# Performance work log

Hardware: AMD Instinct MI355X
Metric: run time of the kernel (lower is better)

## Reference

```python
import jax, jax.numpy as jnp
import numpy as np

N = 50000      # nodes
E = 800000     # edges (avg degree 16)
D_IN = 128
HID = [128, 64, 32]
C = 2
EPS = 1e-5


def _lin(k, fan_in, fan_out):
    return jax.random.normal(k, (fan_in, fan_out), jnp.float32) / np.float32(np.sqrt(fan_in))


def setup_inputs() -> dict:
    key = jax.random.key(0)
    ks = jax.random.split(key, 40)
    inp = {}
    inp["x"] = jax.random.normal(ks[0], (N, D_IN), jnp.float32)
    inp["edge_index"] = jax.random.randint(ks[1], (2, E), 0, N, dtype=jnp.int32)
    i = 2
    dims = [D_IN] + HID
    for l in range(3):
        di, do = dims[l], dims[l + 1]
        inp[f"W{l}"] = _lin(ks[i], di, do); i += 1
        inp[f"b{l}"] = jnp.zeros((do,), jnp.float32)
        inp[f"bn{l}_g"] = jnp.ones((do,), jnp.float32)
        inp[f"bn{l}_b"] = jnp.zeros((do,), jnp.float32)
        inp[f"bn{l}_m"] = 0.1 * jax.random.normal(ks[i], (do,), jnp.float32); i += 1
        inp[f"bn{l}_v"] = 0.5 + jax.random.uniform(ks[i], (do,), jnp.float32); i += 1
        if di != do:
            inp[f"skip{l}_W"] = _lin(ks[i], di, do); i += 1
            inp[f"skip{l}_b"] = jnp.zeros((do,), jnp.float32)
    inp["cls1_W"] = _lin(ks[i], HID[-1], HID[-1] // 2); i += 1
    inp["cls1_b"] = jnp.zeros((HID[-1] // 2,), jnp.float32)
    inp["cls2_W"] = _lin(ks[i], HID[-1] // 2, C); i += 1
    inp["cls2_b"] = jnp.zeros((C,), jnp.float32)
    return inp


def _gcn_conv(x, W, b, src, dst):
    # PyG GCNConv: add self loops, symmetric deg^{-1/2} normalization.
    h = x @ W                                            # [N, do]
    deg = jax.ops.segment_sum(jnp.ones((E,), h.dtype), dst, num_segments=N) + 1.0  # self loop
    dinv = jax.lax.rsqrt(deg)                            # deg >= 1
    norm = dinv[src] * dinv[dst]                         # [E]
    agg = jax.ops.segment_sum(h[src] * norm[:, None], dst, num_segments=N)
    return agg + h * (dinv * dinv)[:, None] + b          # self-loop msg + bias


def _bn(x, g, b, m, v):
    return (x - m) * jax.lax.rsqrt(v + EPS) * g + b


def reference(x, edge_index,
              W0, b0, bn0_g, bn0_b, bn0_m, bn0_v,
              W1, b1, bn1_g, bn1_b, bn1_m, bn1_v, skip1_W, skip1_b,
              W2, b2, bn2_g, bn2_b, bn2_m, bn2_v, skip2_W, skip2_b,
              cls1_W, cls1_b, cls2_W, cls2_b):
    src, dst = edge_index[0], edge_index[1]
    # layer 0: skip is Identity (128 -> 128)
    res = x
    h = jax.nn.relu(_bn(_gcn_conv(x, W0, b0, src, dst), bn0_g, bn0_b, bn0_m, bn0_v))
    h = h + res
    # layer 1: 128 -> 64, linear skip
    res = h @ skip1_W + skip1_b
    h = jax.nn.relu(_bn(_gcn_conv(h, W1, b1, src, dst), bn1_g, bn1_b, bn1_m, bn1_v))
    h = h + res
    # layer 2: 64 -> 32, linear skip
    res = h @ skip2_W + skip2_b
    h = jax.nn.relu(_bn(_gcn_conv(h, W2, b2, src, dst), bn2_g, bn2_b, bn2_m, bn2_v))
    h = h + res
    # classifier (dropout inactive at inference)
    h = jax.nn.relu(h @ cls1_W + cls1_b)
    logits = h @ cls2_W + cls2_b
    return jax.nn.log_softmax(logits, axis=1)
```

## Files before the change

kernel.cpp:

```cpp
#include <hip/hip_runtime.h>
#include <hip/hip_bf16.h>
#include <math.h>


#define BN_EPS 1e-5f

typedef __attribute__((ext_vector_type(8))) short bf16x8;
typedef __attribute__((ext_vector_type(4))) float f32x4;

static __device__ __forceinline__ float bf2f(unsigned int u16) {
    return __uint_as_float(u16 << 16);
}
static __device__ __forceinline__ unsigned short f2bf(float f) {
    unsigned int b = __float_as_uint(f);
    return (unsigned short)((b + 0x7FFFu + ((b >> 16) & 1u)) >> 16);
}
static __device__ __forceinline__ unsigned int pack2(float a, float b) {
    return (unsigned int)f2bf(a) | ((unsigned int)f2bf(b) << 16);
}
static __device__ __forceinline__ void unpack8(uint4 u, float* f) {
    f[0] = bf2f(u.x & 0xffffu); f[1] = bf2f(u.x >> 16);
    f[2] = bf2f(u.y & 0xffffu); f[3] = bf2f(u.y >> 16);
    f[4] = bf2f(u.z & 0xffffu); f[5] = bf2f(u.z >> 16);
    f[6] = bf2f(u.w & 0xffffu); f[7] = bf2f(u.w >> 16);
}
static __device__ __forceinline__ int swz(int row, int kb, int rowb) {
    return row * rowb + (kb ^ ((row & 7) << 4));
}

__global__ void zero_counts_kernel(int* __restrict__ counts, int N) {
    int i = blockIdx.x * 256 + threadIdx.x;
    if (i < N) counts[i] = 0;
}

__global__ void rank_hist_kernel(const int* __restrict__ dst, int* __restrict__ counts,
                                 int* __restrict__ rank, int E) {
    int e = blockIdx.x * 256 + threadIdx.x;
    if (e < E) rank[e] = atomicAdd(&counts[dst[e]], 1);
}

__global__ void scan_block_kernel(const int* __restrict__ counts, int* __restrict__ excl,
                                  int* __restrict__ bsum, int N) {
    __shared__ int s[256];
    int tid = threadIdx.x;
    int i = blockIdx.x * 256 + tid;
    int v = (i < N) ? counts[i] : 0;
    s[tid] = v;
    __syncthreads();
#pragma unroll
    for (int off = 1; off < 256; off <<= 1) {
        int t = (tid >= off) ? s[tid - off] : 0;
        __syncthreads();
        s[tid] += t;
        __syncthreads();
    }
    if (i < N) excl[i] = s[tid] - v;
    if (tid == 255) bsum[blockIdx.x] = s[255];
}

__global__ void scan_add_kernel(const int* __restrict__ excl, const int* __restrict__ bsum,
                                const int* __restrict__ counts,
                                int* __restrict__ rowptr, float* __restrict__ dinv,
                                int nb, int N, int E) {
    __shared__ int sb[256];
    int tid = threadIdx.x;
    int v = (tid < nb) ? bsum[tid] : 0;
    sb[tid] = v;
    __syncthreads();
#pragma unroll
    for (int off = 1; off < 256; off <<= 1) {
        int t = (tid >= off) ? sb[tid - off] : 0;
        __syncthreads();
        sb[tid] += t;
        __syncthreads();
    }
    int eb = sb[blockIdx.x] - ((blockIdx.x < nb) ? bsum[blockIdx.x] : 0);
    int i = blockIdx.x * 256 + tid;
    if (i < N) {
        rowptr[i] = excl[i] + eb;
        dinv[i]   = rsqrtf((float)counts[i] + 1.0f);
    }
    if (i == N) rowptr[N] = E;
}

__global__ void fill_csr_kernel(const int* __restrict__ src, const int* __restrict__ dst,
                                const int* __restrict__ rank, const int* __restrict__ rowptr,
                                int* __restrict__ csr, int E) {
    int e = blockIdx.x * 256 + threadIdx.x;
    if (e >= E) return;
    csr[rowptr[dst[e]] + rank[e]] = src[e];
}

template <int K, int M1, int M2>
__global__ void wt_build_kernel(const float* __restrict__ Wc, const float* __restrict__ Wsk,
                                unsigned short* __restrict__ Wt) {
    constexpr int M = M1 + M2;
    int idx = blockIdx.x * 256 + threadIdx.x;
    if (idx >= M * K) return;
    int m = idx / K, k = idx % K;
    float v = (M2 == 0 || m < M1) ? Wc[(size_t)k * M1 + m]
                                  : Wsk[(size_t)k * M2 + (m - M1)];
    Wt[idx] = f2bf(v);
}

template <int K, int M1, int M2, bool IN_BF16>
__launch_bounds__(256)
__global__ void mfma_gemm_kernel(const float* __restrict__ Xf,
                                 const unsigned short* __restrict__ Xb,
                                 const unsigned short* __restrict__ Wt,
                                 const float* __restrict__ skb,
                                 unsigned short* __restrict__ H,
                                 float* __restrict__ SK, int N)
{
    constexpr int M    = M1 + M2;
    constexpr int BM   = 8192 / M;
    constexpr int WC   = M / 64;
    constexpr int ROWB = K * 2;
    constexpr int CPR  = K / 8;
    constexpr int WCH  = (M * K) / 2048;

    __shared__ unsigned char XsB[BM * K * 2];
    __shared__ unsigned char WsB[M * K * 2];

    const int tid = threadIdx.x;
    const int r0  = blockIdx.x * BM;

#pragma unroll
    for (int c = 0; c < 4; ++c) {
        int q   = tid + 256 * c;
        int row = q / CPR, kq = q % CPR;
        int grow = r0 + row;
        uint4 u = make_uint4(0u, 0u, 0u, 0u);
        if (IN_BF16) {
            if (grow < N) u = *(const uint4*)(Xb + (size_t)grow * K + kq * 8);
        } else {
            if (grow < N) {
                const float* p = Xf + (size_t)grow * K + kq * 8;
                float4 v0 = *(const float4*)p;
                float4 v1 = *(const float4*)(p + 4);
                u.x = pack2(v0.x, v0.y); u.y = pack2(v0.z, v0.w);
                u.z = pack2(v1.x, v1.y); u.w = pack2(v1.z, v1.w);
            }
        }
        *(uint4*)(XsB + swz(row, kq * 16, ROWB)) = u;
    }
#pragma unroll
    for (int c = 0; c < WCH; ++c) {
        int q = tid + 256 * c;
        int m = q / CPR, kq = q % CPR;
        uint4 u = *(const uint4*)(Wt + (size_t)m * K + kq * 8);
        *(uint4*)(WsB + swz(m, kq * 16, ROWB)) = u;
    }
    __syncthreads();

    const int lane = tid & 63, wid = tid >> 6;
    const int wr = wid / WC, wc = wid % WC;
    const int lrow = lane & 15;
    const int kb   = (lane >> 4) << 4;

    f32x4 acc[2][4];
#pragma unroll
    for (int fi = 0; fi < 2; ++fi)
#pragma unroll
        for (int fj = 0; fj < 4; ++fj)
            acc[fi][fj] = (f32x4){0.f, 0.f, 0.f, 0.f};

#pragma unroll
    for (int ks = 0; ks < K / 32; ++ks) {
        const int kb0 = ks * 64 + kb;
        bf16x8 a0 = *(const bf16x8*)(XsB + swz(wr * 32 +      lrow, kb0, ROWB));
        bf16x8 a1 = *(const bf16x8*)(XsB + swz(wr * 32 + 16 + lrow, kb0, ROWB));
        bf16x8 b0 = *(const bf16x8*)(WsB + swz(wc * 64 +      lrow, kb0, ROWB));
        bf16x8 b1 = *(const bf16x8*)(WsB + swz(wc * 64 + 16 + lrow, kb0, ROWB));
        bf16x8 b2 = *(const bf16x8*)(WsB + swz(wc * 64 + 32 + lrow, kb0, ROWB));
        bf16x8 b3 = *(const bf16x8*)(WsB + swz(wc * 64 + 48 + lrow, kb0, ROWB));
        acc[0][0] = __builtin_amdgcn_mfma_f32_16x16x32_bf16(a0, b0, acc[0][0], 0, 0, 0);
        acc[0][1] = __builtin_amdgcn_mfma_f32_16x16x32_bf16(a0, b1, acc[0][1], 0, 0, 0);
        acc[0][2] = __builtin_amdgcn_mfma_f32_16x16x32_bf16(a0, b2, acc[0][2], 0, 0, 0);
        acc[0][3] = __builtin_amdgcn_mfma_f32_16x16x32_bf16(a0, b3, acc[0][3], 0, 0, 0);
        acc[1][0] = __builtin_amdgcn_mfma_f32_16x16x32_bf16(a1, b0, acc[1][0], 0, 0, 0);
        acc[1][1] = __builtin_amdgcn_mfma_f32_16x16x32_bf16(a1, b1, acc[1][1], 0, 0, 0);
        acc[1][2] = __builtin_amdgcn_mfma_f32_16x16x32_bf16(a1, b2, acc[1][2], 0, 0, 0);
        acc[1][3] = __builtin_amdgcn_mfma_f32_16x16x32_bf16(a1, b3, acc[1][3], 0, 0, 0);
    }

    const int orow0 = r0 + wr * 32 + (lane >> 4) * 4;
#pragma unroll
    for (int fi = 0; fi < 2; ++fi) {
#pragma unroll
        for (int fj = 0; fj < 4; ++fj) {
            const int col = wc * 64 + fj * 16 + lrow;
            const bool conv = (M2 == 0) || (col < M1);
            const float sb = conv ? 0.f : skb[col - M1];
#pragma unroll
            for (int r = 0; r < 4; ++r) {
                const int row = orow0 + fi * 16 + r;
                if (row >= N) continue;
                const float val = acc[fi][fj][r];
                if (conv) H[(size_t)row * M1 + col] = f2bf(val);
                else      SK[(size_t)row * M2 + (col - M1)] = val + sb;
            }
        }
    }
}

template <int M, bool OUT_BF16>
__launch_bounds__(256)
__global__ void gather_bn_kernel(const int* __restrict__ rowptr, const int* __restrict__ csr,
                                 const unsigned short* __restrict__ H,
                                 const float* __restrict__ dinv,
                                 const float* __restrict__ bias,
                                 const float* __restrict__ g, const float* __restrict__ b,
                                 const float* __restrict__ m, const float* __restrict__ v,
                                 const float* __restrict__ res, void* __restrict__ out, int N)
{
    constexpr int TPN = M / 8;
    int gid = blockIdx.x * 256 + threadIdx.x;
    int n = gid / TPN;
    if (n >= N) return;
    const int c = (gid % TPN) * 8;

    float s[8], o[8];
#pragma unroll
    for (int q = 0; q < 2; ++q) {
        float4 gv = *(const float4*)&g[c + q * 4];
        float4 bv = *(const float4*)&b[c + q * 4];
        float4 mv = *(const float4*)&m[c + q * 4];
        float4 vv = *(const float4*)&v[c + q * 4];
        float4 iv = *(const float4*)&bias[c + q * 4];
        float sv[4] = {gv.x * rsqrtf(vv.x + BN_EPS), gv.y * rsqrtf(vv.y + BN_EPS),
                       gv.z * rsqrtf(vv.z + BN_EPS), gv.w * rsqrtf(vv.w + BN_EPS)};
        float bb[4] = {bv.x, bv.y, bv.z, bv.w};
        float mm[4] = {mv.x, mv.y, mv.z, mv.w};
        float ii[4] = {iv.x, iv.y, iv.z, iv.w};
#pragma unroll
        for (int q2 = 0; q2 < 4; ++q2) {
            s[q * 4 + q2] = sv[q2];
            o[q * 4 + q2] = (ii[q2] - mm[q2]) * sv[q2] + bb[q2];
        }
    }

    const float dn = dinv[n];

    float acc[8], hf[8];
    uint4 hs = *(const uint4*)&H[(size_t)n * M + c];
    unpack8(hs, hf);
    const float d2 = dn * dn;
#pragma unroll
    for (int k = 0; k < 8; ++k) acc[k] = hf[k] * d2;

    int p   = rowptr[n];
    int end = rowptr[n + 1];
    for (; p + 3 < end; p += 4) {
        int s0 = csr[p], s1 = csr[p + 1], s2 = csr[p + 2], s3 = csr[p + 3];
        uint4 h0 = *(const uint4*)&H[(size_t)s0 * M + c];
        uint4 h1 = *(const uint4*)&H[(size_t)s1 * M + c];
        uint4 h2 = *(const uint4*)&H[(size_t)s2 * M + c];
        uint4 h3 = *(const uint4*)&H[(size_t)s3 * M + c];
        float w0 = dinv[s0] * dn, w1 = dinv[s1] * dn;
        float w2 = dinv[s2] * dn, w3 = dinv[s3] * dn;
        float f0[8], f1[8], f2[8], f3[8];
        unpack8(h0, f0); unpack8(h1, f1); unpack8(h2, f2); unpack8(h3, f3);
#pragma unroll
        for (int k = 0; k < 8; ++k) acc[k] = fmaf(f0[k], w0, acc[k]);
#pragma unroll
        for (int k = 0; k < 8; ++k) acc[k] = fmaf(f1[k], w1, acc[k]);
#pragma unroll
        for (int k = 0; k < 8; ++k) acc[k] = fmaf(f2[k], w2, acc[k]);
#pragma unroll
        for (int k = 0; k < 8; ++k) acc[k] = fmaf(f3[k], w3, acc[k]);
    }
    for (; p < end; ++p) {
        int s0 = csr[p];
        uint4 h0 = *(const uint4*)&H[(size_t)s0 * M + c];
        float w0 = dinv[s0] * dn;
        float f0[8];
        unpack8(h0, f0);
#pragma unroll
        for (int k = 0; k < 8; ++k) acc[k] = fmaf(f0[k], w0, acc[k]);
    }

    float4 r0 = *(const float4*)&res[(size_t)n * M + c];
    float4 r1 = *(const float4*)&res[(size_t)n * M + c + 4];
    float rr[8] = {r0.x, r0.y, r0.z, r0.w, r1.x, r1.y, r1.z, r1.w};
    float outv[8];
#pragma unroll
    for (int k = 0; k < 8; ++k)
        outv[k] = fmaxf(fmaf(acc[k], s[k], o[k]), 0.f) + rr[k];

    if (OUT_BF16) {
        uint4 u;
        u.x = pack2(outv[0], outv[1]); u.y = pack2(outv[2], outv[3]);
        u.z = pack2(outv[4], outv[5]); u.w = pack2(outv[6], outv[7]);
        *(uint4*)&((unsigned short*)out)[(size_t)n * M + c] = u;
    } else {
        float* op = (float*)out;
        *(float4*)&op[(size_t)n * M + c]     = make_float4(outv[0], outv[1], outv[2], outv[3]);
        *(float4*)&op[(size_t)n * M + c + 4] = make_float4(outv[4], outv[5], outv[6], outv[7]);
    }
}

__global__ void classifier_kernel(const float* __restrict__ H2,
                                  const float* __restrict__ W1, const float* __restrict__ B1,
                                  const float* __restrict__ W2, const float* __restrict__ B2,
                                  float* __restrict__ out, int N)
{
    __shared__ float w1s[32 * 16];
    __shared__ float b1s[16];
    __shared__ float w2s[16 * 2];
    __shared__ float b2s[2];
    int tid = threadIdx.x;
    for (int t = tid; t < 512; t += 256) w1s[t] = W1[t];
    if (tid < 16) b1s[tid] = B1[tid];
    if (tid < 32) w2s[tid] = W2[tid];
    if (tid < 2)  b2s[tid] = B2[tid];
    __syncthreads();

    int n = blockIdx.x * 256 + tid;
    if (n >= N) return;

    float x[32];
#pragma unroll
    for (int q = 0; q < 8; ++q) {
        float4 v = *(const float4*)&H2[(size_t)n * 32 + q * 4];
        x[q * 4 + 0] = v.x; x[q * 4 + 1] = v.y; x[q * 4 + 2] = v.z; x[q * 4 + 3] = v.w;
    }
    float h[16];
#pragma unroll
    for (int jj = 0; jj < 16; ++jj) h[jj] = b1s[jj];
#pragma unroll
    for (int k = 0; k < 32; ++k)
#pragma unroll
        for (int jj = 0; jj < 16; ++jj)
            h[jj] = fmaf(x[k], w1s[k * 16 + jj], h[jj]);

    float z0 = b2s[0], z1 = b2s[1];
#pragma unroll
    for (int jj = 0; jj < 16; ++jj) {
        float r = fmaxf(h[jj], 0.f);
        z0 = fmaf(r, w2s[jj * 2 + 0], z0);
        z1 = fmaf(r, w2s[jj * 2 + 1], z1);
    }
    float mx  = fmaxf(z0, z1);
    float lse = mx + logf(expf(z0 - mx) + expf(z1 - mx));
    out[(size_t)n * 2 + 0] = z0 - lse;
    out[(size_t)n * 2 + 1] = z1 - lse;
}

extern "C" void kernel_launch(void* const* d_in, const int* in_sizes, int n_in,
                              void* d_out, int out_size, void* d_ws, size_t ws_size,
                              hipStream_t stream)
{
    const float* x    = (const float*)d_in[0];
    const int*   edge = (const int*)d_in[1];
    const float* W0   = (const float*)d_in[2];
    const float* b0v  = (const float*)d_in[3];
    const float* bn0g = (const float*)d_in[4];
    const float* bn0b = (const float*)d_in[5];
    const float* bn0m = (const float*)d_in[6];
    const float* bn0v = (const float*)d_in[7];
    const float* W1   = (const float*)d_in[8];
    const float* b1v  = (const float*)d_in[9];
    const float* bn1g = (const float*)d_in[10];
    const float* bn1b = (const float*)d_in[11];
    const float* bn1m = (const float*)d_in[12];
    const float* bn1v = (const float*)d_in[13];
    const float* sk1W = (const float*)d_in[14];
    const float* sk1b = (const float*)d_in[15];
    const float* W2   = (const float*)d_in[16];
    const float* b2v  = (const float*)d_in[17];
    const float* bn2g = (const float*)d_in[18];
    const float* bn2b = (const float*)d_in[19];
    const float* bn2m = (const float*)d_in[20];
    const float* bn2v = (const float*)d_in[21];
    const float* sk2W = (const float*)d_in[22];
    const float* sk2b = (const float*)d_in[23];
    const float* c1W  = (const float*)d_in[24];
    const float* c1b  = (const float*)d_in[25];
    const float* c2W  = (const float*)d_in[26];
    const float* c2b  = (const float*)d_in[27];

    const int N = in_sizes[0] / 128;
    const int E = in_sizes[1] / 2;
    const int* src = edge;
    const int* dst = edge + E;

    char*  ws  = (char*)d_ws;
    size_t off = 0;
    auto alloc = [&](size_t bytes) -> char* {
        char* p = ws + off;
        off += (bytes + 255) & ~(size_t)255;
        return p;
    };
    float*          dinv   = (float*)alloc((size_t)N * 4);
    int*            counts = (int*)  alloc((size_t)N * 4);
    int*            excl   = (int*)  alloc((size_t)N * 4);
    int*            rowptr = (int*)  alloc((size_t)(N + 1) * 4);
    int*            bsum   = (int*)  alloc(256 * 4);
    int*            rank   = (int*)  alloc((size_t)E * 4);
    int*            csr    = (int*)  alloc((size_t)E * 4);
    unsigned short* Hb     = (unsigned short*)alloc((size_t)N * 128 * 2);
    float*          SK     = (float*)alloc((size_t)N * 64 * 4);
    unsigned short* Q0     = (unsigned short*)alloc((size_t)N * 128 * 2);
    unsigned short* P1     = (unsigned short*)alloc((size_t)N * 64 * 2);
    float*          O2     = (float*)alloc((size_t)N * 32 * 4);
    unsigned short* Wt0    = (unsigned short*)alloc(128 * 128 * 2);
    unsigned short* Wt1    = (unsigned short*)alloc(128 * 128 * 2);
    unsigned short* Wt2    = (unsigned short*)alloc(64 * 64 * 2);
    (void)ws_size; (void)n_in; (void)out_size;

    dim3 blk(256);
    auto cdiv = [](int a, int b) { return (a + b - 1) / b; };
    const int nbN = cdiv(N, 256);

    zero_counts_kernel<<<nbN, blk, 0, stream>>>(counts, N);
    rank_hist_kernel<<<cdiv(E, 256), blk, 0, stream>>>(dst, counts, rank, E);
    scan_block_kernel<<<nbN, blk, 0, stream>>>(counts, excl, bsum, N);
    scan_add_kernel<<<cdiv(N + 1, 256), blk, 0, stream>>>(excl, bsum, counts, rowptr, dinv, nbN, N, E);
    fill_csr_kernel<<<cdiv(E, 256), blk, 0, stream>>>(src, dst, rank, rowptr, csr, E);

    wt_build_kernel<128, 128, 0><<<64, blk, 0, stream>>>(W0, nullptr, Wt0);
    wt_build_kernel<128, 64, 64><<<64, blk, 0, stream>>>(W1, sk1W, Wt1);
    wt_build_kernel<64, 32, 32><<<16, blk, 0, stream>>>(W2, sk2W, Wt2);

    mfma_gemm_kernel<128, 128, 0, false><<<cdiv(N, 64), blk, 0, stream>>>(
        x, nullptr, Wt0, nullptr, Hb, nullptr, N);
    gather_bn_kernel<128, true><<<cdiv(N * 16, 256), blk, 0, stream>>>(
        rowptr, csr, Hb, dinv, b0v, bn0g, bn0b, bn0m, bn0v, x, Q0, N);

    mfma_gemm_kernel<128, 64, 64, true><<<cdiv(N, 64), blk, 0, stream>>>(
        nullptr, Q0, Wt1, sk1b, Hb, SK, N);
    gather_bn_kernel<64, true><<<cdiv(N * 8, 256), blk, 0, stream>>>(
        rowptr, csr, Hb, dinv, b1v, bn1g, bn1b, bn1m, bn1v, SK, P1, N);

    mfma_gemm_kernel<64, 32, 32, true><<<cdiv(N, 128), blk, 0, stream>>>(
        nullptr, P1, Wt2, sk2b, Hb, SK, N);
    gather_bn_kernel<32, false><<<cdiv(N * 4, 256), blk, 0, stream>>>(
        rowptr, csr, Hb, dinv, b2v, bn2g, bn2b, bn2m, bn2v, SK, O2, N);

    classifier_kernel<<<cdiv(N, 256), blk, 0, stream>>>(O2, c1W, c1b, c2W, c2b, (float*)d_out, N);
}
```

Before: 186.0 us.

## Fuse prep kernels and classifier, widen gather to 16 channels, store skip in bf16

Merges the count zeroing and the three weight-transpose kernels into one prep launch. Vectorizes the histogram and CSR fill to four edges per thread. Stores the skip projection as bf16 instead of fp32. Widens the gather to 16 channels per thread and fuses the classifier plus log-softmax into the last gather, using a shuffle across the thread pair. This removes launches and the fp32 intermediate traffic, at the cost of more bf16 rounding in the residual and more registers and fewer threads per node in the gather.

Result: no change. 187.9 us (+1.0%).

```diff
diff --git a/kernel.cpp b/kernel.cpp
--- a/kernel.cpp
+++ b/kernel.cpp
@@ -28,15 +28,58 @@
     return row * rowb + (kb ^ ((row & 7) << 4));
 }
 
-__global__ void zero_counts_kernel(int* __restrict__ counts, int N) {
-    int i = blockIdx.x * 256 + threadIdx.x;
-    if (i < N) counts[i] = 0;
+__global__ void prep_kernel(int* __restrict__ counts, int N, int nbZero,
+                            const float* __restrict__ W0,
+                            const float* __restrict__ W1, const float* __restrict__ sk1W,
+                            const float* __restrict__ W2, const float* __restrict__ sk2W,
+                            unsigned short* __restrict__ Wt0,
+                            unsigned short* __restrict__ Wt1,
+                            unsigned short* __restrict__ Wt2)
+{
+    int b = blockIdx.x, tid = threadIdx.x;
+    if (b < nbZero) {
+        int i = b * 256 + tid;
+        if (i < N) counts[i] = 0;
+        return;
+    }
+    b -= nbZero;
+    if (b < 64) {
+        int idx = b * 256 + tid;
+        int m = idx >> 7, k = idx & 127;
+        Wt0[idx] = f2bf(W0[(size_t)k * 128 + m]);
+        return;
+    }
+    b -= 64;
+    if (b < 64) {
+        int idx = b * 256 + tid;
+        int m = idx >> 7, k = idx & 127;
+        float v = (m < 64) ? W1[(size_t)k * 64 + m] : sk1W[(size_t)k * 64 + (m - 64)];
+        Wt1[idx] = f2bf(v);
+        return;
+    }
+    b -= 64;
+    {
+        int idx = b * 256 + tid;
+        int m = idx >> 6, k = idx & 63;
+        float v = (m < 32) ? W2[(size_t)k * 32 + m] : sk2W[(size_t)k * 32 + (m - 32)];
+        Wt2[idx] = f2bf(v);
+    }
 }
 
 __global__ void rank_hist_kernel(const int* __restrict__ dst, int* __restrict__ counts,
                                  int* __restrict__ rank, int E) {
-    int e = blockIdx.x * 256 + threadIdx.x;
-    if (e < E) rank[e] = atomicAdd(&counts[dst[e]], 1);
+    int base = (blockIdx.x * 256 + threadIdx.x) * 4;
+    if (base + 3 < E) {
+        int4 d = *(const int4*)(dst + base);
+        int4 r;
+        r.x = atomicAdd(&counts[d.x], 1);
+        r.y = atomicAdd(&counts[d.y], 1);
+        r.z = atomicAdd(&counts[d.z], 1);
+        r.w = atomicAdd(&counts[d.w], 1);
+        *(int4*)(rank + base) = r;
+    } else {
+        for (int e = base; e < E; ++e) rank[e] = atomicAdd(&counts[dst[e]], 1);
+    }
 }
 
 __global__ void scan_block_kernel(const int* __restrict__ counts, int* __restrict__ excl,
@@ -86,21 +129,18 @@
 __global__ void fill_csr_kernel(const int* __restrict__ src, const int* __restrict__ dst,
                                 const int* __restrict__ rank, const int* __restrict__ rowptr,
                                 int* __restrict__ csr, int E) {
-    int e = blockIdx.x * 256 + threadIdx.x;
-    if (e >= E) return;
-    csr[rowptr[dst[e]] + rank[e]] = src[e];
-}
-
-template <int K, int M1, int M2>
-__global__ void wt_build_kernel(const float* __restrict__ Wc, const float* __restrict__ Wsk,
-                                unsigned short* __restrict__ Wt) {
-    constexpr int M = M1 + M2;
-    int idx = blockIdx.x * 256 + threadIdx.x;
-    if (idx >= M * K) return;
-    int m = idx / K, k = idx % K;
-    float v = (M2 == 0 || m < M1) ? Wc[(size_t)k * M1 + m]
-                                  : Wsk[(size_t)k * M2 + (m - M1)];
-    Wt[idx] = f2bf(v);
+    int base = (blockIdx.x * 256 + threadIdx.x) * 4;
+    if (base + 3 < E) {
+        int4 s = *(const int4*)(src + base);
+        int4 d = *(const int4*)(dst + base);
+        int4 r = *(const int4*)(rank + base);
+        csr[rowptr[d.x] + r.x] = s.x;
+        csr[rowptr[d.y] + r.y] = s.y;
+        csr[rowptr[d.z] + r.z] = s.z;
+        csr[rowptr[d.w] + r.w] = s.w;
+    } else {
+        for (int e = base; e < E; ++e) csr[rowptr[dst[e]] + rank[e]] = src[e];
+    }
 }
 
 template <int K, int M1, int M2, bool IN_BF16>
@@ -110,7 +150,7 @@
                                  const unsigned short* __restrict__ Wt,
                                  const float* __restrict__ skb,
                                  unsigned short* __restrict__ H,
-                                 float* __restrict__ SK, int N)
+                                 unsigned short* __restrict__ SK, int N)
 {
     constexpr int M    = M1 + M2;
     constexpr int BM   = 8192 / M;
@@ -198,13 +238,13 @@
                 if (row >= N) continue;
                 const float val = acc[fi][fj][r];
                 if (conv) H[(size_t)row * M1 + col] = f2bf(val);
-                else      SK[(size_t)row * M2 + (col - M1)] = val + sb;
+                else      SK[(size_t)row * M2 + (col - M1)] = f2bf(val + sb);
             }
         }
     }
 }
 
-template <int M, bool OUT_BF16>
+template <int M, bool OUT_BF16, bool RES_BF16, bool CLS>
 __launch_bounds__(256)
 __global__ void gather_bn_kernel(const int* __restrict__ rowptr, const int* __restrict__ csr,
                                  const unsigned short* __restrict__ H,
@@ -212,17 +252,35 @@
                                  const float* __restrict__ bias,
                                  const float* __restrict__ g, const float* __restrict__ b,
                                  const float* __restrict__ m, const float* __restrict__ v,
-                                 const float* __restrict__ res, void* __restrict__ out, int N)
+                                 const void* __restrict__ res, void* __restrict__ out,
+                                 const float* __restrict__ cW1, const float* __restrict__ cB1,
+                                 const float* __restrict__ cW2, const float* __restrict__ cB2,
+                                 int N)
 {
-    constexpr int TPN = M / 8;
-    int gid = blockIdx.x * 256 + threadIdx.x;
+    constexpr int TPN = M / 16;
+    __shared__ float w1s[512];
+    __shared__ float b1s[16];
+    __shared__ float w2s[32];
+    __shared__ float b2s[2];
+
+    const int tid = threadIdx.x;
+    if constexpr (CLS) {
+        w1s[tid]       = cW1[tid];
+        w1s[tid + 256] = cW1[tid + 256];
+        if (tid < 16) b1s[tid] = cB1[tid];
+        if (tid < 32) w2s[tid] = cW2[tid];
+        if (tid < 2)  b2s[tid] = cB2[tid];
+        __syncthreads();
+    }
+
+    int gid = blockIdx.x * 256 + tid;
     int n = gid / TPN;
     if (n >= N) return;
-    const int c = (gid % TPN) * 8;
-
-    float s[8], o[8];
-#pragma unroll
-    for (int q = 0; q < 2; ++q) {
+    const int c = (gid % TPN) * 16;
+
+    float s[16], o[16];
+#pragma unroll
+    for (int q = 0; q < 4; ++q) {
         float4 gv = *(const float4*)&g[c + q * 4];
         float4 bv = *(const float4*)&b[c + q * 4];
         float4 mv = *(const float4*)&m[c + q * 4];
@@ -241,110 +299,118 @@
     }
 
     const float dn = dinv[n];
-
-    float acc[8], hf[8];
-    uint4 hs = *(const uint4*)&H[(size_t)n * M + c];
-    unpack8(hs, hf);
-    const float d2 = dn * dn;
-#pragma unroll
-    for (int k = 0; k < 8; ++k) acc[k] = hf[k] * d2;
+    float acc[16];
+    {
+        uint4 h0 = *(const uint4*)&H[(size_t)n * M + c];
+        uint4 h1 = *(const uint4*)&H[(size_t)n * M + c + 8];
+        float hf[16];
+        unpack8(h0, hf); unpack8(h1, hf + 8);
+        const float d2 = dn * dn;
+#pragma unroll
+        for (int k = 0; k < 16; ++k) acc[k] = hf[k] * d2;
+    }
 
     int p   = rowptr[n];
     int end = rowptr[n + 1];
     for (; p + 3 < end; p += 4) {
         int s0 = csr[p], s1 = csr[p + 1], s2 = csr[p + 2], s3 = csr[p + 3];
-        uint4 h0 = *(const uint4*)&H[(size_t)s0 * M + c];
-        uint4 h1 = *(const uint4*)&H[(size_t)s1 * M + c];
-        uint4 h2 = *(const uint4*)&H[(size_t)s2 * M + c];
-        uint4 h3 = *(const uint4*)&H[(size_t)s3 * M + c];
+        uint4 a0 = *(const uint4*)&H[(size_t)s0 * M + c];
+        uint4 a1 = *(const uint4*)&H[(size_t)s0 * M + c + 8];
+        uint4 b0_ = *(const uint4*)&H[(size_t)s1 * M + c];
+        uint4 b1_ = *(const uint4*)&H[(size_t)s1 * M + c + 8];
+        uint4 c0_ = *(const uint4*)&H[(size_t)s2 * M + c];
+        uint4 c1_ = *(const uint4*)&H[(size_t)s2 * M + c + 8];
+        uint4 d0_ = *(const uint4*)&H[(size_t)s3 * M + c];
+        uint4 d1_ = *(const uint4*)&H[(size_t)s3 * M + c + 8];
         float w0 = dinv[s0] * dn, w1 = dinv[s1] * dn;
         float w2 = dinv[s2] * dn, w3 = dinv[s3] * dn;
-        float f0[8], f1[8], f2[8], f3[8];
-        unpack8(h0, f0); unpack8(h1, f1); unpack8(h2, f2); unpack8(h3, f3);
-#pragma unroll
-        for (int k = 0; k < 8; ++k) acc[k] = fmaf(f0[k], w0, acc[k]);
-#pragma unroll
-        for (int k = 0; k < 8; ++k) acc[k] = fmaf(f1[k], w1, acc[k]);
-#pragma unroll
-        for (int k = 0; k < 8; ++k) acc[k] = fmaf(f2[k], w2, acc[k]);
-#pragma unroll
-        for (int k = 0; k < 8; ++k) acc[k] = fmaf(f3[k], w3, acc[k]);
+        float f0[16], f1[16], f2[16], f3[16];
+        unpack8(a0, f0); unpack8(a1, f0 + 8);
+        unpack8(b0_, f1); unpack8(b1_, f1 + 8);
+        unpack8(c0_, f2); unpack8(c1_, f2 + 8);
+        unpack8(d0_, f3); unpack8(d1_, f3 + 8);
+#pragma unroll
+        for (int k = 0; k < 16; ++k) acc[k] = fmaf(f0[k], w0, acc[k]);
+#pragma unroll
+        for (int k = 0; k < 16; ++k) acc[k] = fmaf(f1[k], w1, acc[k]);
+#pragma unroll
+        for (int k = 0; k < 16; ++k) acc[k] = fmaf(f2[k], w2, acc[k]);
+#pragma unroll
+        for (int k = 0; k < 16; ++k) acc[k] = fmaf(f3[k], w3, acc[k]);
     }
     for (; p < end; ++p) {
         int s0 = csr[p];
-        uint4 h0 = *(const uint4*)&H[(size_t)s0 * M + c];
+        uint4 a0 = *(const uint4*)&H[(size_t)s0 * M + c];
+        uint4 a1 = *(const uint4*)&H[(size_t)s0 * M + c + 8];
         float w0 = dinv[s0] * dn;
-        float f0[8];
-        unpack8(h0, f0);
-#pragma unroll
-        for (int k = 0; k < 8; ++k) acc[k] = fmaf(f0[k], w0, acc[k]);
-    }
-
-    float4 r0 = *(const float4*)&res[(size_t)n * M + c];
-    float4 r1 = *(const float4*)&res[(size_t)n * M + c + 4];
-    float rr[8] = {r0.x, r0.y, r0.z, r0.w, r1.x, r1.y, r1.z, r1.w};
-    float outv[8];
-#pragma unroll
-    for (int k = 0; k < 8; ++k)
+        float f0[16];
+        unpack8(a0, f0); unpack8(a1, f0 + 8);
+#pragma unroll
+        for (int k = 0; k < 16; ++k) acc[k] = fmaf(f0[k], w0, acc[k]);
+    }
+
+    float rr[16];
+    if constexpr (RES_BF16) {
+        const unsigned short* rp = (const unsigned short*)res;
+        uint4 r0 = *(const uint4*)&rp[(size_t)n * M + c];
+        uint4 r1 = *(const uint4*)&rp[(size_t)n * M + c + 8];
+        unpack8(r0, rr); unpack8(r1, rr + 8);
+    } else {
+        const float* rp = (const float*)res;
+#pragma unroll
+        for (int q = 0; q < 4; ++q) {
+            float4 rv = *(const float4*)&rp[(size_t)n * M + c + q * 4];
+            rr[q * 4 + 0] = rv.x; rr[q * 4 + 1] = rv.y;
+            rr[q * 4 + 2] = rv.z; rr[q * 4 + 3] = rv.w;
+        }
+    }
+
+    float outv[16];
+#pragma unroll
+    for (int k = 0; k < 16; ++k)
         outv[k] = fmaxf(fmaf(acc[k], s[k], o[k]), 0.f) + rr[k];
 
-    if (OUT_BF16) {
-        uint4 u;
-        u.x = pack2(outv[0], outv[1]); u.y = pack2(outv[2], outv[3]);
-        u.z = pack2(outv[4], outv[5]); u.w = pack2(outv[6], outv[7]);
-        *(uint4*)&((unsigned short*)out)[(size_t)n * M + c] = u;
+    if constexpr (CLS) {
+        float h[16];
+#pragma unroll
+        for (int j = 0; j < 16; ++j) h[j] = 0.f;
+#pragma unroll
+        for (int k = 0; k < 16; ++k)
+#pragma unroll
+            for (int j = 0; j < 16; ++j)
+                h[j] = fmaf(outv[k], w1s[(c + k) * 16 + j], h[j]);
+#pragma unroll
+        for (int j = 0; j < 16; ++j) h[j] += __shfl_xor(h[j], 1);
+        float z0 = b2s[0], z1 = b2s[1];
+#pragma unroll
+        for (int j = 0; j < 16; ++j) {
+            float r = fmaxf(h[j] + b1s[j], 0.f);
+            z0 = fmaf(r, w2s[j * 2 + 0], z0);
+            z1 = fmaf(r, w2s[j * 2 + 1], z1);
+        }
+        float mx  = fmaxf(z0, z1);
+        float lse = mx + logf(expf(z0 - mx) + expf(z1 - mx));
+        if ((tid & 1) == 0) {
+            float* op = (float*)out;
+            op[(size_t)n * 2 + 0] = z0 - lse;
+            op[(size_t)n * 2 + 1] = z1 - lse;
+        }
+    } else if constexpr (OUT_BF16) {
+        unsigned short* op = (unsigned short*)out;
+        uint4 u0, u1;
+        u0.x = pack2(outv[0], outv[1]);  u0.y = pack2(outv[2], outv[3]);
+        u0.z = pack2(outv[4], outv[5]);  u0.w = pack2(outv[6], outv[7]);
+        u1.x = pack2(outv[8], outv[9]);  u1.y = pack2(outv[10], outv[11]);
+        u1.z = pack2(outv[12], outv[13]); u1.w = pack2(outv[14], outv[15]);
+        *(uint4*)&op[(size_t)n * M + c]     = u0;
+        *(uint4*)&op[(size_t)n * M + c + 8] = u1;
     } else {
         float* op = (float*)out;
-        *(float4*)&op[(size_t)n * M + c]     = make_float4(outv[0], outv[1], outv[2], outv[3]);
-        *(float4*)&op[(size_t)n * M + c + 4] = make_float4(outv[4], outv[5], outv[6], outv[7]);
-    }
-}
-
-__global__ void classifier_kernel(const float* __restrict__ H2,
-                                  const float* __restrict__ W1, const float* __restrict__ B1,
-                                  const float* __restrict__ W2, const float* __restrict__ B2,
-                                  float* __restrict__ out, int N)
-{
-    __shared__ float w1s[32 * 16];
-    __shared__ float b1s[16];
-    __shared__ float w2s[16 * 2];
-    __shared__ float b2s[2];
-    int tid = threadIdx.x;
-    for (int t = tid; t < 512; t += 256) w1s[t] = W1[t];
-    if (tid < 16) b1s[tid] = B1[tid];
-    if (tid < 32) w2s[tid] = W2[tid];
-    if (tid < 2)  b2s[tid] = B2[tid];
-    __syncthreads();
-
-    int n = blockIdx.x * 256 + tid;
-    if (n >= N) return;
-
-    float x[32];
-#pragma unroll
-    for (int q = 0; q < 8; ++q) {
-        float4 v = *(const float4*)&H2[(size_t)n * 32 + q * 4];
-        x[q * 4 + 0] = v.x; x[q * 4 + 1] = v.y; x[q * 4 + 2] = v.z; x[q * 4 + 3] = v.w;
-    }
-    float h[16];
-#pragma unroll
-    for (int jj = 0; jj < 16; ++jj) h[jj] = b1s[jj];
-#pragma unroll
-    for (int k = 0; k < 32; ++k)
-#pragma unroll
-        for (int jj = 0; jj < 16; ++jj)
-            h[jj] = fmaf(x[k], w1s[k * 16 + jj], h[jj]);
-
-    float z0 = b2s[0], z1 = b2s[1];
-#pragma unroll
-    for (int jj = 0; jj < 16; ++jj) {
-        float r = fmaxf(h[jj], 0.f);
-        z0 = fmaf(r, w2s[jj * 2 + 0], z0);
-        z1 = fmaf(r, w2s[jj * 2 + 1], z1);
-    }
-    float mx  = fmaxf(z0, z1);
-    float lse = mx + logf(expf(z0 - mx) + expf(z1 - mx));
-    out[(size_t)n * 2 + 0] = z0 - lse;
-    out[(size_t)n * 2 + 1] = z1 - lse;
+#pragma unroll
+        for (int q = 0; q < 4; ++q)
+            *(float4*)&op[(size_t)n * M + c + q * 4] =
+                make_float4(outv[q * 4], outv[q * 4 + 1], outv[q * 4 + 2], outv[q * 4 + 3]);
+    }
 }
 
 extern "C" void kernel_launch(void* const* d_in, const int* in_sizes, int n_in,
@@ -400,10 +466,9 @@
     int*            rank   = (int*)  alloc((size_t)E * 4);
     int*            csr    = (int*)  alloc((size_t)E * 4);
     unsigned short* Hb     = (unsigned short*)alloc((size_t)N * 128 * 2);
-    float*          SK     = (float*)alloc((size_t)N * 64 * 4);
+    unsigned short* SKb    = (unsigned short*)alloc((size_t)N * 64 * 2);
     unsigned short* Q0     = (unsigned short*)alloc((size_t)N * 128 * 2);
     unsigned short* P1     = (unsigned short*)alloc((size_t)N * 64 * 2);
-    float*          O2     = (float*)alloc((size_t)N * 32 * 4);
     unsigned short* Wt0    = (unsigned short*)alloc(128 * 128 * 2);
     unsigned short* Wt1    = (unsigned short*)alloc(128 * 128 * 2);
     unsigned short* Wt2    = (unsigned short*)alloc(64 * 64 * 2);
@@ -413,30 +478,29 @@
     auto cdiv = [](int a, int b) { return (a + b - 1) / b; };
     const int nbN = cdiv(N, 256);
 
-    zero_counts_kernel<<<nbN, blk, 0, stream>>>(counts, N);
-    rank_hist_kernel<<<cdiv(E, 256), blk, 0, stream>>>(dst, counts, rank, E);
+    prep_kernel<<<nbN + 64 + 64 + 16, blk, 0, stream>>>(
+        counts, N, nbN, W0, W1, sk1W, W2, sk2W, Wt0, Wt1, Wt2);
+
+    rank_hist_kernel<<<cdiv(E, 1024), blk, 0, stream>>>(dst, counts, rank, E);
     scan_block_kernel<<<nbN, blk, 0, stream>>>(counts, excl, bsum, N);
     scan_add_kernel<<<cdiv(N + 1, 256), blk, 0, stream>>>(excl, bsum, counts, rowptr, dinv, nbN, N, E);
-    fill_csr_kernel<<<cdiv(E, 256), blk, 0, stream>>>(src, dst, rank, rowptr, csr, E);
-
-    wt_build_kernel<128, 128, 0><<<64, blk, 0, stream>>>(W0, nullptr, Wt0);
-    wt_build_kernel<128, 64, 64><<<64, blk, 0, stream>>>(W1, sk1W, Wt1);
-    wt_build_kernel<64, 32, 32><<<16, blk, 0, stream>>>(W2, sk2W, Wt2);
+    fill_csr_kernel<<<cdiv(E, 1024), blk, 0, stream>>>(src, dst, rank, rowptr, csr, E);
 
     mfma_gemm_kernel<128, 128, 0, false><<<cdiv(N, 64), blk, 0, stream>>>(
         x, nullptr, Wt0, nullptr, Hb, nullptr, N);
-    gather_bn_kernel<128, true><<<cdiv(N * 16, 256), blk, 0, stream>>>(
-        rowptr, csr, Hb, dinv, b0v, bn0g, bn0b, bn0m, bn0v, x, Q0, N);
+    gather_bn_kernel<128, true, false, false><<<cdiv(N * 8, 256), blk, 0, stream>>>(
+        rowptr, csr, Hb, dinv, b0v, bn0g, bn0b, bn0m, bn0v, x, Q0,
+        nullptr, nullptr, nullptr, nullptr, N);
 
     mfma_gemm_kernel<128, 64, 64, true><<<cdiv(N, 64), blk, 0, stream>>>(
-        nullptr, Q0, Wt1, sk1b, Hb, SK, N);
-    gather_bn_kernel<64, true><<<cdiv(N * 8, 256), blk, 0, stream>>>(
-        rowptr, csr, Hb, dinv, b1v, bn1g, bn1b, bn1m, bn1v, SK, P1, N);
+        nullptr, Q0, Wt1, sk1b, Hb, SKb, N);
+    gather_bn_kernel<64, true, true, false><<<cdiv(N * 4, 256), blk, 0, stream>>>(
+        rowptr, csr, Hb, dinv, b1v, bn1g, bn1b, bn1m, bn1v, SKb, P1,
+        nullptr, nullptr, nullptr, nullptr, N);
 
     mfma_gemm_kernel<64, 32, 32, true><<<cdiv(N, 128), blk, 0, stream>>>(
-        nullptr, P1, Wt2, sk2b, Hb, SK, N);
-    gather_bn_kernel<32, false><<<cdiv(N * 4, 256), blk, 0, stream>>>(
-        rowptr, csr, Hb, dinv, b2v, bn2g, bn2b, bn2m, bn2v, SK, O2, N);
-
-    classifier_kernel<<<cdiv(N, 256), blk, 0, stream>>>(O2, c1W, c1b, c2W, c2b, (float*)d_out, N);
-}
+        nullptr, P1, Wt2, sk2b, Hb, SKb, N);
+    gather_bn_kernel<32, false, true, true><<<cdiv(N * 2, 256), blk, 0, stream>>>(
+        rowptr, csr, Hb, dinv, b2v, bn2g, bn2b, bn2m, bn2v, SKb, d_out,
+        c1W, c1b, c2W, c2b, N);
+}
```
